# Kernel optimization log

Hardware: AMD Instinct MI355X
Metric: run time of the kernel (lower is better)

The kernel has to match this reference:

```python
import jax, jax.numpy as jnp
import numpy as np

NEG_BIG = -9e15


def setup_inputs() -> dict:
    key = jax.random.key(0)
    k1, k2, k3, k4 = jax.random.split(key, 4)
    B, N, F_in, F_out = 8, 2048, 512, 256
    x = jax.random.normal(k1, (B, N, F_in), dtype=jnp.float32)
    adj = jax.random.randint(k2, (B, N, N), 0, 2, dtype=jnp.int32)
    W = jax.random.normal(k3, (F_in, F_out), dtype=jnp.float32) * (1.414 / np.sqrt(F_in))
    a = jax.random.normal(k4, (2 * F_out, 1), dtype=jnp.float32) * 0.1
    return {"x": x, "adj": adj, "W": W, "a": a}


def reference(x, adj, W, a):
    # x: [B,N,Fin], adj: [B,N,N] int mask, W: [Fin,Fout], a: [2*Fout,1]
    alpha = 0.2  # LeakyReLU negative slope
    F_out = W.shape[1]
    h = jnp.einsum('bnf,fo->bno', x, W)              # [B,N,Fout]
    a1 = a[:F_out, 0]                                # [Fout]
    a2 = a[F_out:, 0]                                # [Fout]
    # e_ij = LeakyReLU([h_i || h_j] . a) = LeakyReLU(h_i.a1 + h_j.a2)
    f = h @ a1                                       # [B,N]
    g = h @ a2                                       # [B,N]
    e = jax.nn.leaky_relu(f[:, :, None] + g[:, None, :], negative_slope=alpha)  # [B,N,N]
    e = jnp.where(adj > 0, e, NEG_BIG)
    attention = jax.nn.softmax(e, axis=2)            # row-wise over neighbors j
    h_prime = jnp.einsum('bij,bjo->bio', attention, h)  # [B,N,Fout]
    return jax.nn.elu(h_prime)                       # concat=True path
```

## Files before the change

### kernel.cpp

```cpp
#include <hip/hip_runtime.h>
#include <hip/hip_bf16.h>
#include <math.h>

#define BATCH 8
#define NN    2048
#define FIN   512
#define FOUT  256
#define NEG_BIG -9000000000000000.0f

typedef __attribute__((ext_vector_type(8))) short bf16x8;
typedef __attribute__((ext_vector_type(4))) float f32x4;

__device__ __forceinline__ unsigned short f2bf(float x) {
    return __bfloat16_as_ushort(__float2bfloat16(x));
}
__device__ __forceinline__ float bf2f(unsigned short h) {
    return __uint_as_float(((unsigned)h) << 16);
}
__device__ __forceinline__ void gload_lds16(const void* g, void* l) {
    __builtin_amdgcn_global_load_lds((const __attribute__((address_space(1))) void*)g,
                                     (__attribute__((address_space(3))) void*)l,
                                     16, 0, 0);
}
__device__ __forceinline__ void lds_barrier() {
    asm volatile("s_waitcnt lgkmcnt(0)" ::: "memory");
    __builtin_amdgcn_s_barrier();
    asm volatile("" ::: "memory");
}

__global__ __launch_bounds__(256) void wt_prep(const float* __restrict__ W,
                                               unsigned short* __restrict__ Wtf_hi,
                                               unsigned short* __restrict__ Wtf_lo) {
    const int tg = blockIdx.x * 256 + threadIdx.x;
    const int n  = tg >> 7;
    const int k4 = (tg & 127) * 4;
    unsigned short h[4], lo[4];
    #pragma unroll
    for (int i = 0; i < 4; i++) {
        const float v = W[(size_t)(k4 + i) * FOUT + n];
        h[i]  = f2bf(v);
        lo[i] = f2bf(v - bf2f(h[i]));
    }
    const int ktile = k4 >> 5;
    const int ntile = n >> 4;
    const int lane  = ((k4 >> 3) & 3) * 16 + (n & 15);
    const size_t daddr = ((size_t)(ktile * 16 + ntile) * 64 + lane) * 8 + (k4 & 7);
    uint2 ph, pl;
    ph.x = h[0]  | ((unsigned)h[1]  << 16); ph.y = h[2]  | ((unsigned)h[3]  << 16);
    pl.x = lo[0] | ((unsigned)lo[1] << 16); pl.y = lo[2] | ((unsigned)lo[3] << 16);
    *(uint2*)(Wtf_hi + daddr) = ph;
    *(uint2*)(Wtf_lo + daddr) = pl;
}

__global__ __launch_bounds__(256, 2) void gemm_xw(const float* __restrict__ x,
        const unsigned short* __restrict__ Wtf_hi,
        const unsigned short* __restrict__ Wtf_lo,
        unsigned short* __restrict__ ht_hi,
        unsigned short* __restrict__ ht_lo) {
    __shared__ unsigned short As_hi[128][40];
    __shared__ unsigned short As_lo[128][40];
    __shared__ __attribute__((aligned(16))) unsigned short Tr[64][136];
    const int t  = threadIdx.x;
    const int m0 = (blockIdx.x >> 2) * 128;
    const int n0 = (blockIdx.x & 3) * 64;
    const int l  = t & 63, w = t >> 6;
    const int wr = w >> 1, wc = w & 1;
    const int lr = l & 15, lk = l >> 4;

    f32x4 acc[4][2];
    #pragma unroll
    for (int mt = 0; mt < 4; mt++)
        #pragma unroll
        for (int nt = 0; nt < 2; nt++) acc[mt][nt] = (f32x4){0.f,0.f,0.f,0.f};

    for (int k0 = 0; k0 < FIN; k0 += 32) {
        float4 xv[4];
        #pragma unroll
        for (int r = 0; r < 4; r++) {
            const int fidx = t + 256*r, m = fidx >> 3, kq = fidx & 7;
            xv[r] = *(const float4*)(x + (size_t)(m0 + m) * FIN + k0 + kq*4);
        }
        bf16x8 bh[2], bl[2];
        const size_t fb = ((size_t)((k0 >> 5) * 16 + (n0 >> 4) + wc*2) * 64 + l) * 8;
        #pragma unroll
        for (int nt = 0; nt < 2; nt++) {
            bh[nt] = *(const bf16x8*)(Wtf_hi + fb + (size_t)nt * 512);
            bl[nt] = *(const bf16x8*)(Wtf_lo + fb + (size_t)nt * 512);
        }
        __syncthreads();
        #pragma unroll
        for (int r = 0; r < 4; r++) {
            const int fidx = t + 256*r, m = fidx >> 3, kq = fidx & 7;
            const float vv[4] = {xv[r].x, xv[r].y, xv[r].z, xv[r].w};
            unsigned short h[4], lo[4];
            #pragma unroll
            for (int i = 0; i < 4; i++) { h[i] = f2bf(vv[i]); lo[i] = f2bf(vv[i] - bf2f(h[i])); }
            uint2 ph, pl;
            ph.x = h[0]  | ((unsigned)h[1]  << 16); ph.y = h[2]  | ((unsigned)h[3]  << 16);
            pl.x = lo[0] | ((unsigned)lo[1] << 16); pl.y = lo[2] | ((unsigned)lo[3] << 16);
            *(uint2*)&As_hi[m][kq*4] = ph;
            *(uint2*)&As_lo[m][kq*4] = pl;
        }
        __syncthreads();
        bf16x8 ah[4], al[4];
        #pragma unroll
        for (int mt = 0; mt < 4; mt++) {
            const int row = wr*64 + mt*16 + lr;
            ah[mt] = *(const bf16x8*)&As_hi[row][lk*8];
            al[mt] = *(const bf16x8*)&As_lo[row][lk*8];
        }
        #pragma unroll
        for (int nt = 0; nt < 2; nt++)
            #pragma unroll
            for (int mt = 0; mt < 4; mt++)
                acc[mt][nt] = __builtin_amdgcn_mfma_f32_16x16x32_bf16(ah[mt], bh[nt], acc[mt][nt], 0, 0, 0);
        #pragma unroll
        for (int nt = 0; nt < 2; nt++)
            #pragma unroll
            for (int mt = 0; mt < 4; mt++)
                acc[mt][nt] = __builtin_amdgcn_mfma_f32_16x16x32_bf16(ah[mt], bl[nt], acc[mt][nt], 0, 0, 0);
        #pragma unroll
        for (int nt = 0; nt < 2; nt++)
            #pragma unroll
            for (int mt = 0; mt < 4; mt++)
                acc[mt][nt] = __builtin_amdgcn_mfma_f32_16x16x32_bf16(al[mt], bh[nt], acc[mt][nt], 0, 0, 0);
    }

    const int bb  = m0 >> 11;
    const int jj0 = m0 & 2047;
    for (int pass = 0; pass < 2; pass++) {
        #pragma unroll
        for (int mt = 0; mt < 4; mt++)
            #pragma unroll
            for (int nt = 0; nt < 2; nt++) {
                const int nl = wc*32 + nt*16 + lr;
                const int ml = wr*64 + mt*16 + lk*4;
                const float vv[4] = {acc[mt][nt].x, acc[mt][nt].y, acc[mt][nt].z, acc[mt][nt].w};
                unsigned short s[4];
                #pragma unroll
                for (int r = 0; r < 4; r++) {
                    const unsigned short hh = f2bf(vv[r]);
                    s[r] = pass ? f2bf(vv[r] - bf2f(hh)) : hh;
                }
                *(unsigned*)&Tr[nl][ml]     = s[0] | ((unsigned)s[1] << 16);
                *(unsigned*)&Tr[nl][ml + 2] = s[2] | ((unsigned)s[3] << 16);
            }
        __syncthreads();
        unsigned short* dst = pass ? ht_lo : ht_hi;
        #pragma unroll
        for (int q = 0; q < 4; q++) {
            const int idx = t + 256*q, row = idx >> 4, c = idx & 15;
            *(uint4*)(dst + ((size_t)(bb * FOUT + n0 + row)) * NN + jj0 + c*8) =
                *(const uint4*)&Tr[row][c*8];
        }
        __syncthreads();
    }
}

__global__ __launch_bounds__(256) void fg2(const unsigned short* __restrict__ ht_hi,
                                           const unsigned short* __restrict__ ht_lo,
                                           const float* __restrict__ a,
                                           float* __restrict__ f, float* __restrict__ g) {
    __shared__ float Fp[4][64], Gp[4][64];
    const int lane = threadIdx.x & 63, wv = threadIdx.x >> 6;
    const int chunk = blockIdx.x;
    const int b  = chunk >> 5;
    const int jw = (chunk & 31) * 64 + lane;
    const size_t base = (size_t)b * FOUT * NN + jw;
    float fs = 0.f, gs = 0.f;
    #pragma unroll 4
    for (int n = wv*64; n < wv*64 + 64; n++) {
        const float hv = bf2f(ht_hi[base + (size_t)n * NN]) + bf2f(ht_lo[base + (size_t)n * NN]);
        fs = fmaf(hv, a[n], fs);
        gs = fmaf(hv, a[FOUT + n], gs);
    }
    Fp[wv][lane] = fs; Gp[wv][lane] = gs;
    __syncthreads();
    if (wv == 0) {
        f[b * NN + jw] = Fp[0][lane] + Fp[1][lane] + Fp[2][lane] + Fp[3][lane];
        g[b * NN + jw] = Gp[0][lane] + Gp[1][lane] + Gp[2][lane] + Gp[3][lane];
    }
}

__global__ __launch_bounds__(512, 1) void gat_attn(
        const unsigned short* __restrict__ ht_hi,
        const unsigned short* __restrict__ ht_lo,
        const int* __restrict__ adj,
        const float* __restrict__ f, const float* __restrict__ g,
        float* __restrict__ out) {
    __shared__ __attribute__((aligned(16))) unsigned short Hs_hi[2][16384];
    __shared__ __attribute__((aligned(16))) unsigned short Hs_lo[2][16384];
    __shared__ __attribute__((aligned(16))) unsigned short Ps_hi[4096];
    __shared__ __attribute__((aligned(16))) unsigned short Ps_lo[4096];
    __shared__ __attribute__((aligned(16))) float fac_s[64];
    __shared__ __attribute__((aligned(16))) float l_s[64];

    const int b  = blockIdx.x & 7;
    const int i0 = (blockIdx.x >> 3) * 64;
    const int t  = threadIdx.x;
    const int w  = t >> 6, l = t & 63;
    const int lr = l & 15, lk = l >> 4;
    const int wr = w >> 2, wc = w & 3;
    const int ar = t >> 3, jg = t & 7;

    const unsigned short* hb_hi = ht_hi + (size_t)b * FOUT * NN;
    const unsigned short* hb_lo = ht_lo + (size_t)b * FOUT * NN;
    const int*   adjr = adj + ((size_t)(b * NN + i0 + ar)) * NN + jg * 8;
    const float* gb   = g + b * NN + jg * 8;
    const float  fi   = f[b * NN + i0 + ar];

    float m_r = -INFINITY, l_r = 0.f;
    f32x4 acc[2][4] = {};
    const int slot = w * 4;

    int4 a0v, a1v; float4 g0v, g1v;

    auto STAGE = [&](int jt) {
        const int buf = jt & 1, j0 = jt * 64;
        #pragma unroll
        for (int q = 0; q < 4; q++) {
            const int idx = (slot + q) * 64 + l;
            const int n = idx >> 3, c = idx & 7;
            const int cc = c ^ (n & 7);
            const size_t go = (size_t)n * NN + j0 + cc * 8;
            gload_lds16(hb_hi + go, &Hs_hi[buf][(slot + q) * 512]);
            gload_lds16(hb_lo + go, &Hs_lo[buf][(slot + q) * 512]);
        }
    };
    auto LOADAG = [&](int jt) {
        const size_t jo = (size_t)jt * 64;
        a0v = *(const int4*)(adjr + jo);
        a1v = *(const int4*)(adjr + jo + 4);
        g0v = *(const float4*)(gb + jo);
        g1v = *(const float4*)(gb + jo + 4);
    };

    STAGE(0);
    asm volatile("" ::: "memory");
    LOADAG(0);

    for (int jt = 0; jt < 32; jt++) {
        const int buf = jt & 1;
        if (jt + 1 < 32) STAGE(jt + 1);
        asm volatile("" ::: "memory");

        {
            float p[8];
            {
                const float v0 = fi + g0v.x, v1 = fi + g0v.y, v2 = fi + g0v.z, v3 = fi + g0v.w;
                const float v4 = fi + g1v.x, v5 = fi + g1v.y, v6 = fi + g1v.z, v7 = fi + g1v.w;
                p[0] = a0v.x > 0 ? (v0 > 0.f ? v0 : 0.2f*v0) : NEG_BIG;
                p[1] = a0v.y > 0 ? (v1 > 0.f ? v1 : 0.2f*v1) : NEG_BIG;
                p[2] = a0v.z > 0 ? (v2 > 0.f ? v2 : 0.2f*v2) : NEG_BIG;
                p[3] = a0v.w > 0 ? (v3 > 0.f ? v3 : 0.2f*v3) : NEG_BIG;
                p[4] = a1v.x > 0 ? (v4 > 0.f ? v4 : 0.2f*v4) : NEG_BIG;
                p[5] = a1v.y > 0 ? (v5 > 0.f ? v5 : 0.2f*v5) : NEG_BIG;
                p[6] = a1v.z > 0 ? (v6 > 0.f ? v6 : 0.2f*v6) : NEG_BIG;
                p[7] = a1v.w > 0 ? (v7 > 0.f ? v7 : 0.2f*v7) : NEG_BIG;
            }
            float mloc = p[0];
            #pragma unroll
            for (int e = 1; e < 8; e++) mloc = fmaxf(mloc, p[e]);
            mloc = fmaxf(mloc, __shfl_xor(mloc, 1));
            mloc = fmaxf(mloc, __shfl_xor(mloc, 2));
            mloc = fmaxf(mloc, __shfl_xor(mloc, 4));
            const float mn = fmaxf(m_r, mloc);
            float rs = 0.f;
            #pragma unroll
            for (int e = 0; e < 8; e++) { p[e] = __expf(p[e] - mn); rs += p[e]; }
            rs += __shfl_xor(rs, 1);
            rs += __shfl_xor(rs, 2);
            rs += __shfl_xor(rs, 4);
            const float fac = __expf(m_r - mn);
            l_r = l_r * fac + rs;
            m_r = mn;
            if (jg == 0) { fac_s[ar] = fac; l_s[ar] = l_r; }
            unsigned hw_[4], lw_[4];
            #pragma unroll
            for (int e = 0; e < 8; e += 2) {
                const unsigned short h0 = f2bf(p[e]),   h1 = f2bf(p[e+1]);
                const unsigned short q0 = f2bf(p[e]   - bf2f(h0));
                const unsigned short q1 = f2bf(p[e+1] - bf2f(h1));
                hw_[e >> 1] = h0 | ((unsigned)h1 << 16);
                lw_[e >> 1] = q0 | ((unsigned)q1 << 16);
            }
            const int cs = (jg ^ (ar & 7)) * 8;
            *(uint4*)&Ps_hi[ar * 64 + cs] = make_uint4(hw_[0], hw_[1], hw_[2], hw_[3]);
            *(uint4*)&Ps_lo[ar * 64 + cs] = make_uint4(lw_[0], lw_[1], lw_[2], lw_[3]);
        }

        if (jt + 1 < 32) LOADAG(jt + 1);

        lds_barrier();

        #pragma unroll
        for (int mt = 0; mt < 2; mt++) {
            const f32x4 fac4 = *(const f32x4*)&fac_s[wr*32 + mt*16 + lk*4];
            #pragma unroll
            for (int nt = 0; nt < 4; nt++) acc[mt][nt] *= fac4;
        }
        __builtin_amdgcn_s_setprio(1);
        #pragma unroll
        for (int kt = 0; kt < 2; kt++) {
            bf16x8 ah[2], al[2], bh[4], bl[4];
            #pragma unroll
            for (int mt = 0; mt < 2; mt++) {
                const int row = wr*32 + mt*16 + lr;
                const int cs  = ((kt*4 + lk) ^ (row & 7)) * 8;
                ah[mt] = *(const bf16x8*)&Ps_hi[row * 64 + cs];
                al[mt] = *(const bf16x8*)&Ps_lo[row * 64 + cs];
            }
            #pragma unroll
            for (int nt = 0; nt < 4; nt++) {
                const int n  = wc*64 + nt*16 + lr;
                const int cs = ((kt*4 + lk) ^ (n & 7)) * 8;
                bh[nt] = *(const bf16x8*)&Hs_hi[buf][n * 64 + cs];
                bl[nt] = *(const bf16x8*)&Hs_lo[buf][n * 64 + cs];
            }
            #pragma unroll
            for (int nt = 0; nt < 4; nt++)
                #pragma unroll
                for (int mt = 0; mt < 2; mt++)
                    acc[mt][nt] = __builtin_amdgcn_mfma_f32_16x16x32_bf16(ah[mt], bh[nt], acc[mt][nt], 0, 0, 0);
            #pragma unroll
            for (int nt = 0; nt < 4; nt++)
                #pragma unroll
                for (int mt = 0; mt < 2; mt++)
                    acc[mt][nt] = __builtin_amdgcn_mfma_f32_16x16x32_bf16(ah[mt], bl[nt], acc[mt][nt], 0, 0, 0);
            #pragma unroll
            for (int nt = 0; nt < 4; nt++)
                #pragma unroll
                for (int mt = 0; mt < 2; mt++)
                    acc[mt][nt] = __builtin_amdgcn_mfma_f32_16x16x32_bf16(al[mt], bh[nt], acc[mt][nt], 0, 0, 0);
        }
        __builtin_amdgcn_s_setprio(0);

        lds_barrier();
    }

    #pragma unroll
    for (int mt = 0; mt < 2; mt++) {
        const f32x4 lv = *(const f32x4*)&l_s[wr*32 + mt*16 + lk*4];
        const float li[4] = {1.f/lv.x, 1.f/lv.y, 1.f/lv.z, 1.f/lv.w};
        #pragma unroll
        for (int nt = 0; nt < 4; nt++) {
            const int n = wc*64 + nt*16 + lr;
            const float av[4] = {acc[mt][nt].x, acc[mt][nt].y, acc[mt][nt].z, acc[mt][nt].w};
            #pragma unroll
            for (int r = 0; r < 4; r++) {
                float v = av[r] * li[r];
                v = v > 0.f ? v : (__expf(v) - 1.f);
                out[((size_t)(b * NN + i0 + wr*32 + mt*16 + lk*4 + r)) * FOUT + n] = v;
            }
        }
    }
}

extern "C" void kernel_launch(void* const* d_in, const int* in_sizes, int n_in,
                              void* d_out, int out_size, void* d_ws, size_t ws_size,
                              hipStream_t stream) {
    const float* x   = (const float*)d_in[0];
    const int*   adj = (const int*)  d_in[1];
    const float* W   = (const float*)d_in[2];
    const float* a   = (const float*)d_in[3];
    float* outp = (float*)d_out;

    char* ws = (char*)d_ws;
    unsigned short* ht_hi  = (unsigned short*)ws;                      ws += (size_t)BATCH*FOUT*NN*2;
    unsigned short* ht_lo  = (unsigned short*)ws;                      ws += (size_t)BATCH*FOUT*NN*2;
    unsigned short* Wtf_hi = (unsigned short*)ws;                      ws += (size_t)FOUT*FIN*2;
    unsigned short* Wtf_lo = (unsigned short*)ws;                      ws += (size_t)FOUT*FIN*2;
    float* f = (float*)ws;                                             ws += (size_t)BATCH*NN*4;
    float* g = (float*)ws;

    wt_prep <<<128, 256, 0, stream>>>(W, Wtf_hi, Wtf_lo);
    gemm_xw <<<512, 256, 0, stream>>>(x, Wtf_hi, Wtf_lo, ht_hi, ht_lo);
    fg2     <<<256, 256, 0, stream>>>(ht_hi, ht_lo, a, f, g);
    gat_attn<<<256, 512, 0, stream>>>(ht_hi, ht_lo, adj, f, g, outp);
}
```

Baseline: 287.3 us.

## Fuse f/g projection into GEMM epilogue and software-pipeline attention loop

The separate fg2 kernel is removed. f and g are now computed in the gemm_xw epilogue through shuffle reductions and atomicAdds into buffers zeroed by a memset. gemm_xw also loads x straight from global memory into MFMA fragments and drops the LDS staging and its barriers. The attention kernel is restructured so that the softmax phase for the next tile overlaps the MFMA work on the current tile, using an explicit vmcnt wait and a hoisted P fragment load. The atomics make the f/g sums order-dependent, and reading x without LDS staging may cost extra global traffic.

Result: slower. 299.4 us (+4.2%).

```diff
diff --git a/kernel.cpp b/kernel.cpp
--- a/kernel.cpp
+++ b/kernel.cpp
@@ -41,8 +41,7 @@
         h[i]  = f2bf(v);
         lo[i] = f2bf(v - bf2f(h[i]));
     }
-    const int ktile = k4 >> 5;
-    const int ntile = n >> 4;
+    const int ktile = k4 >> 5, ntile = n >> 4;
     const int lane  = ((k4 >> 3) & 3) * 16 + (n & 15);
     const size_t daddr = ((size_t)(ktile * 16 + ntile) * 64 + lane) * 8 + (k4 & 7);
     uint2 ph, pl;
@@ -55,10 +54,10 @@
 __global__ __launch_bounds__(256, 2) void gemm_xw(const float* __restrict__ x,
         const unsigned short* __restrict__ Wtf_hi,
         const unsigned short* __restrict__ Wtf_lo,
+        const float* __restrict__ a,
         unsigned short* __restrict__ ht_hi,
-        unsigned short* __restrict__ ht_lo) {
-    __shared__ unsigned short As_hi[128][40];
-    __shared__ unsigned short As_lo[128][40];
+        unsigned short* __restrict__ ht_lo,
+        float* __restrict__ f, float* __restrict__ g) {
     __shared__ __attribute__((aligned(16))) unsigned short Tr[64][136];
     const int t  = threadIdx.x;
     const int m0 = (blockIdx.x >> 2) * 128;
@@ -73,13 +72,9 @@
         #pragma unroll
         for (int nt = 0; nt < 2; nt++) acc[mt][nt] = (f32x4){0.f,0.f,0.f,0.f};
 
+    const float* xw = x + (size_t)(m0 + wr*64 + lr) * FIN + lk*8;
+
     for (int k0 = 0; k0 < FIN; k0 += 32) {
-        float4 xv[4];
-        #pragma unroll
-        for (int r = 0; r < 4; r++) {
-            const int fidx = t + 256*r, m = fidx >> 3, kq = fidx & 7;
-            xv[r] = *(const float4*)(x + (size_t)(m0 + m) * FIN + k0 + kq*4);
-        }
         bf16x8 bh[2], bl[2];
         const size_t fb = ((size_t)((k0 >> 5) * 16 + (n0 >> 4) + wc*2) * 64 + l) * 8;
         #pragma unroll
@@ -87,27 +82,18 @@
             bh[nt] = *(const bf16x8*)(Wtf_hi + fb + (size_t)nt * 512);
             bl[nt] = *(const bf16x8*)(Wtf_lo + fb + (size_t)nt * 512);
         }
-        __syncthreads();
-        #pragma unroll
-        for (int r = 0; r < 4; r++) {
-            const int fidx = t + 256*r, m = fidx >> 3, kq = fidx & 7;
-            const float vv[4] = {xv[r].x, xv[r].y, xv[r].z, xv[r].w};
-            unsigned short h[4], lo[4];
-            #pragma unroll
-            for (int i = 0; i < 4; i++) { h[i] = f2bf(vv[i]); lo[i] = f2bf(vv[i] - bf2f(h[i])); }
-            uint2 ph, pl;
-            ph.x = h[0]  | ((unsigned)h[1]  << 16); ph.y = h[2]  | ((unsigned)h[3]  << 16);
-            pl.x = lo[0] | ((unsigned)lo[1] << 16); pl.y = lo[2] | ((unsigned)lo[3] << 16);
-            *(uint2*)&As_hi[m][kq*4] = ph;
-            *(uint2*)&As_lo[m][kq*4] = pl;
-        }
-        __syncthreads();
         bf16x8 ah[4], al[4];
         #pragma unroll
         for (int mt = 0; mt < 4; mt++) {
-            const int row = wr*64 + mt*16 + lr;
-            ah[mt] = *(const bf16x8*)&As_hi[row][lk*8];
-            al[mt] = *(const bf16x8*)&As_lo[row][lk*8];
+            const float4 v0 = *(const float4*)(xw + (size_t)mt*16*FIN + k0);
+            const float4 v1 = *(const float4*)(xw + (size_t)mt*16*FIN + k0 + 4);
+            const float vv[8] = {v0.x,v0.y,v0.z,v0.w,v1.x,v1.y,v1.z,v1.w};
+            #pragma unroll
+            for (int e = 0; e < 8; e++) {
+                const unsigned short hh = f2bf(vv[e]);
+                ah[mt][e] = (short)hh;
+                al[mt][e] = (short)f2bf(vv[e] - bf2f(hh));
+            }
         }
         #pragma unroll
         for (int nt = 0; nt < 2; nt++)
@@ -128,6 +114,32 @@
 
     const int bb  = m0 >> 11;
     const int jj0 = m0 & 2047;
+
+    {
+        const int nA = n0 + wc*32 + lr;
+        const float a1A = a[nA],        a1B = a[nA + 16];
+        const float a2A = a[FOUT + nA], a2B = a[FOUT + nA + 16];
+        #pragma unroll
+        for (int mt = 0; mt < 4; mt++) {
+            #pragma unroll
+            for (int r = 0; r < 4; r++) {
+                float fp = acc[mt][0][r] * a1A + acc[mt][1][r] * a1B;
+                float gp = acc[mt][0][r] * a2A + acc[mt][1][r] * a2B;
+                #pragma unroll
+                for (int m = 1; m < 16; m <<= 1) {
+                    fp += __shfl_xor(fp, m);
+                    gp += __shfl_xor(gp, m);
+                }
+                if (lr == 0) {
+                    const int row = m0 + wr*64 + mt*16 + lk*4 + r;
+                    const int jj  = row & 2047;
+                    atomicAdd(&f[(size_t)bb * NN + jj], fp);
+                    atomicAdd(&g[(size_t)bb * NN + jj], gp);
+                }
+            }
+        }
+    }
+
     for (int pass = 0; pass < 2; pass++) {
         #pragma unroll
         for (int mt = 0; mt < 4; mt++)
@@ -154,31 +166,6 @@
                 *(const uint4*)&Tr[row][c*8];
         }
         __syncthreads();
-    }
-}
-
-__global__ __launch_bounds__(256) void fg2(const unsigned short* __restrict__ ht_hi,
-                                           const unsigned short* __restrict__ ht_lo,
-                                           const float* __restrict__ a,
-                                           float* __restrict__ f, float* __restrict__ g) {
-    __shared__ float Fp[4][64], Gp[4][64];
-    const int lane = threadIdx.x & 63, wv = threadIdx.x >> 6;
-    const int chunk = blockIdx.x;
-    const int b  = chunk >> 5;
-    const int jw = (chunk & 31) * 64 + lane;
-    const size_t base = (size_t)b * FOUT * NN + jw;
-    float fs = 0.f, gs = 0.f;
-    #pragma unroll 4
-    for (int n = wv*64; n < wv*64 + 64; n++) {
-        const float hv = bf2f(ht_hi[base + (size_t)n * NN]) + bf2f(ht_lo[base + (size_t)n * NN]);
-        fs = fmaf(hv, a[n], fs);
-        gs = fmaf(hv, a[FOUT + n], gs);
-    }
-    Fp[wv][lane] = fs; Gp[wv][lane] = gs;
-    __syncthreads();
-    if (wv == 0) {
-        f[b * NN + jw] = Fp[0][lane] + Fp[1][lane] + Fp[2][lane] + Fp[3][lane];
-        g[b * NN + jw] = Gp[0][lane] + Gp[1][lane] + Gp[2][lane] + Gp[3][lane];
     }
 }
 
@@ -234,82 +221,54 @@
         g0v = *(const float4*)(gb + jo);
         g1v = *(const float4*)(gb + jo + 4);
     };
-
-    STAGE(0);
-    asm volatile("" ::: "memory");
-    LOADAG(0);
-
-    for (int jt = 0; jt < 32; jt++) {
-        const int buf = jt & 1;
-        if (jt + 1 < 32) STAGE(jt + 1);
-        asm volatile("" ::: "memory");
-
+    auto PHASE_A = [&]() {
+        float p[8];
         {
-            float p[8];
-            {
-                const float v0 = fi + g0v.x, v1 = fi + g0v.y, v2 = fi + g0v.z, v3 = fi + g0v.w;
-                const float v4 = fi + g1v.x, v5 = fi + g1v.y, v6 = fi + g1v.z, v7 = fi + g1v.w;
-                p[0] = a0v.x > 0 ? (v0 > 0.f ? v0 : 0.2f*v0) : NEG_BIG;
-                p[1] = a0v.y > 0 ? (v1 > 0.f ? v1 : 0.2f*v1) : NEG_BIG;
-                p[2] = a0v.z > 0 ? (v2 > 0.f ? v2 : 0.2f*v2) : NEG_BIG;
-                p[3] = a0v.w > 0 ? (v3 > 0.f ? v3 : 0.2f*v3) : NEG_BIG;
-                p[4] = a1v.x > 0 ? (v4 > 0.f ? v4 : 0.2f*v4) : NEG_BIG;
-                p[5] = a1v.y > 0 ? (v5 > 0.f ? v5 : 0.2f*v5) : NEG_BIG;
-                p[6] = a1v.z > 0 ? (v6 > 0.f ? v6 : 0.2f*v6) : NEG_BIG;
-                p[7] = a1v.w > 0 ? (v7 > 0.f ? v7 : 0.2f*v7) : NEG_BIG;
-            }
-            float mloc = p[0];
-            #pragma unroll
-            for (int e = 1; e < 8; e++) mloc = fmaxf(mloc, p[e]);
-            mloc = fmaxf(mloc, __shfl_xor(mloc, 1));
-            mloc = fmaxf(mloc, __shfl_xor(mloc, 2));
-            mloc = fmaxf(mloc, __shfl_xor(mloc, 4));
-            const float mn = fmaxf(m_r, mloc);
-            float rs = 0.f;
-            #pragma unroll
-            for (int e = 0; e < 8; e++) { p[e] = __expf(p[e] - mn); rs += p[e]; }
-            rs += __shfl_xor(rs, 1);
-            rs += __shfl_xor(rs, 2);
-            rs += __shfl_xor(rs, 4);
-            const float fac = __expf(m_r - mn);
-            l_r = l_r * fac + rs;
-            m_r = mn;
-            if (jg == 0) { fac_s[ar] = fac; l_s[ar] = l_r; }
-            unsigned hw_[4], lw_[4];
-            #pragma unroll
-            for (int e = 0; e < 8; e += 2) {
-                const unsigned short h0 = f2bf(p[e]),   h1 = f2bf(p[e+1]);
-                const unsigned short q0 = f2bf(p[e]   - bf2f(h0));
-                const unsigned short q1 = f2bf(p[e+1] - bf2f(h1));
-                hw_[e >> 1] = h0 | ((unsigned)h1 << 16);
-                lw_[e >> 1] = q0 | ((unsigned)q1 << 16);
-            }
-            const int cs = (jg ^ (ar & 7)) * 8;
-            *(uint4*)&Ps_hi[ar * 64 + cs] = make_uint4(hw_[0], hw_[1], hw_[2], hw_[3]);
-            *(uint4*)&Ps_lo[ar * 64 + cs] = make_uint4(lw_[0], lw_[1], lw_[2], lw_[3]);
-        }
-
-        if (jt + 1 < 32) LOADAG(jt + 1);
-
-        lds_barrier();
-
-        #pragma unroll
-        for (int mt = 0; mt < 2; mt++) {
-            const f32x4 fac4 = *(const f32x4*)&fac_s[wr*32 + mt*16 + lk*4];
-            #pragma unroll
-            for (int nt = 0; nt < 4; nt++) acc[mt][nt] *= fac4;
-        }
-        __builtin_amdgcn_s_setprio(1);
+            const float v0 = fi + g0v.x, v1 = fi + g0v.y, v2 = fi + g0v.z, v3 = fi + g0v.w;
+            const float v4 = fi + g1v.x, v5 = fi + g1v.y, v6 = fi + g1v.z, v7 = fi + g1v.w;
+            p[0] = a0v.x > 0 ? (v0 > 0.f ? v0 : 0.2f*v0) : NEG_BIG;
+            p[1] = a0v.y > 0 ? (v1 > 0.f ? v1 : 0.2f*v1) : NEG_BIG;
+            p[2] = a0v.z > 0 ? (v2 > 0.f ? v2 : 0.2f*v2) : NEG_BIG;
+            p[3] = a0v.w > 0 ? (v3 > 0.f ? v3 : 0.2f*v3) : NEG_BIG;
+            p[4] = a1v.x > 0 ? (v4 > 0.f ? v4 : 0.2f*v4) : NEG_BIG;
+            p[5] = a1v.y > 0 ? (v5 > 0.f ? v5 : 0.2f*v5) : NEG_BIG;
+            p[6] = a1v.z > 0 ? (v6 > 0.f ? v6 : 0.2f*v6) : NEG_BIG;
+            p[7] = a1v.w > 0 ? (v7 > 0.f ? v7 : 0.2f*v7) : NEG_BIG;
+        }
+        float mloc = p[0];
+        #pragma unroll
+        for (int e = 1; e < 8; e++) mloc = fmaxf(mloc, p[e]);
+        mloc = fmaxf(mloc, __shfl_xor(mloc, 1));
+        mloc = fmaxf(mloc, __shfl_xor(mloc, 2));
+        mloc = fmaxf(mloc, __shfl_xor(mloc, 4));
+        const float mn = fmaxf(m_r, mloc);
+        float rs = 0.f;
+        #pragma unroll
+        for (int e = 0; e < 8; e++) { p[e] = __expf(p[e] - mn); rs += p[e]; }
+        rs += __shfl_xor(rs, 1);
+        rs += __shfl_xor(rs, 2);
+        rs += __shfl_xor(rs, 4);
+        const float fac = __expf(m_r - mn);
+        l_r = l_r * fac + rs;
+        m_r = mn;
+        if (jg == 0) { fac_s[ar] = fac; l_s[ar] = l_r; }
+        unsigned hw_[4], lw_[4];
+        #pragma unroll
+        for (int e = 0; e < 8; e += 2) {
+            const unsigned short h0 = f2bf(p[e]),   h1 = f2bf(p[e+1]);
+            const unsigned short q0 = f2bf(p[e]   - bf2f(h0));
+            const unsigned short q1 = f2bf(p[e+1] - bf2f(h1));
+            hw_[e >> 1] = h0 | ((unsigned)h1 << 16);
+            lw_[e >> 1] = q0 | ((unsigned)q1 << 16);
+        }
+        const int cs = (jg ^ (ar & 7)) * 8;
+        *(uint4*)&Ps_hi[ar * 64 + cs] = make_uint4(hw_[0], hw_[1], hw_[2], hw_[3]);
+        *(uint4*)&Ps_lo[ar * 64 + cs] = make_uint4(lw_[0], lw_[1], lw_[2], lw_[3]);
+    };
+    auto MFMA_TILE = [&](int buf, const bf16x8 (&ahf)[2][2], const bf16x8 (&alf)[2][2]) {
         #pragma unroll
         for (int kt = 0; kt < 2; kt++) {
-            bf16x8 ah[2], al[2], bh[4], bl[4];
-            #pragma unroll
-            for (int mt = 0; mt < 2; mt++) {
-                const int row = wr*32 + mt*16 + lr;
-                const int cs  = ((kt*4 + lk) ^ (row & 7)) * 8;
-                ah[mt] = *(const bf16x8*)&Ps_hi[row * 64 + cs];
-                al[mt] = *(const bf16x8*)&Ps_lo[row * 64 + cs];
-            }
+            bf16x8 bh[4], bl[4];
             #pragma unroll
             for (int nt = 0; nt < 4; nt++) {
                 const int n  = wc*64 + nt*16 + lr;
@@ -321,21 +280,76 @@
             for (int nt = 0; nt < 4; nt++)
                 #pragma unroll
                 for (int mt = 0; mt < 2; mt++)
-                    acc[mt][nt] = __builtin_amdgcn_mfma_f32_16x16x32_bf16(ah[mt], bh[nt], acc[mt][nt], 0, 0, 0);
+                    acc[mt][nt] = __builtin_amdgcn_mfma_f32_16x16x32_bf16(ahf[mt][kt], bh[nt], acc[mt][nt], 0, 0, 0);
             #pragma unroll
             for (int nt = 0; nt < 4; nt++)
                 #pragma unroll
                 for (int mt = 0; mt < 2; mt++)
-                    acc[mt][nt] = __builtin_amdgcn_mfma_f32_16x16x32_bf16(ah[mt], bl[nt], acc[mt][nt], 0, 0, 0);
+                    acc[mt][nt] = __builtin_amdgcn_mfma_f32_16x16x32_bf16(ahf[mt][kt], bl[nt], acc[mt][nt], 0, 0, 0);
             #pragma unroll
             for (int nt = 0; nt < 4; nt++)
                 #pragma unroll
                 for (int mt = 0; mt < 2; mt++)
-                    acc[mt][nt] = __builtin_amdgcn_mfma_f32_16x16x32_bf16(al[mt], bh[nt], acc[mt][nt], 0, 0, 0);
-        }
-        __builtin_amdgcn_s_setprio(0);
-
+                    acc[mt][nt] = __builtin_amdgcn_mfma_f32_16x16x32_bf16(alf[mt][kt], bh[nt], acc[mt][nt], 0, 0, 0);
+        }
+    };
+
+    STAGE(0);
+    LOADAG(0);
+    PHASE_A();
+    LOADAG(1);
+    lds_barrier();
+
+    bf16x8 ahf[2][2], alf[2][2];
+    f32x4 fac4[2];
+
+    for (int jt = 0; jt < 31; jt++) {
+        const int buf = jt & 1;
+        STAGE(jt + 1);
+        asm volatile("s_waitcnt vmcnt(8)" ::: "memory");
+        __builtin_amdgcn_sched_barrier(0);
+        #pragma unroll
+        for (int mt = 0; mt < 2; mt++) {
+            fac4[mt] = *(const f32x4*)&fac_s[wr*32 + mt*16 + lk*4];
+            #pragma unroll
+            for (int kt = 0; kt < 2; kt++) {
+                const int row = wr*32 + mt*16 + lr;
+                const int cs  = ((kt*4 + lk) ^ (row & 7)) * 8;
+                ahf[mt][kt] = *(const bf16x8*)&Ps_hi[row * 64 + cs];
+                alf[mt][kt] = *(const bf16x8*)&Ps_lo[row * 64 + cs];
+            }
+        }
         lds_barrier();
+        #pragma unroll
+        for (int mt = 0; mt < 2; mt++)
+            #pragma unroll
+            for (int nt = 0; nt < 4; nt++) acc[mt][nt] *= fac4[mt];
+        PHASE_A();
+        if (jt < 30) LOADAG(jt + 2);
+        MFMA_TILE(buf, ahf, alf);
+        lds_barrier();
+    }
+
+    {
+        asm volatile("s_waitcnt vmcnt(0)" ::: "memory");
+        __builtin_amdgcn_sched_barrier(0);
+        #pragma unroll
+        for (int mt = 0; mt < 2; mt++) {
+            fac4[mt] = *(const f32x4*)&fac_s[wr*32 + mt*16 + lk*4];
+            #pragma unroll
+            for (int kt = 0; kt < 2; kt++) {
+                const int row = wr*32 + mt*16 + lr;
+                const int cs  = ((kt*4 + lk) ^ (row & 7)) * 8;
+                ahf[mt][kt] = *(const bf16x8*)&Ps_hi[row * 64 + cs];
+                alf[mt][kt] = *(const bf16x8*)&Ps_lo[row * 64 + cs];
+            }
+        }
+        lds_barrier();
+        #pragma unroll
+        for (int mt = 0; mt < 2; mt++)
+            #pragma unroll
+            for (int nt = 0; nt < 4; nt++) acc[mt][nt] *= fac4[mt];
+        MFMA_TILE(1, ahf, alf);
     }
 
     #pragma unroll
@@ -373,8 +387,8 @@
     float* f = (float*)ws;                                             ws += (size_t)BATCH*NN*4;
     float* g = (float*)ws;
 
+    hipMemsetAsync(f, 0, (size_t)2 * BATCH * NN * 4, stream);
     wt_prep <<<128, 256, 0, stream>>>(W, Wtf_hi, Wtf_lo);
-    gemm_xw <<<512, 256, 0, stream>>>(x, Wtf_hi, Wtf_lo, ht_hi, ht_lo);
-    fg2     <<<256, 256, 0, stream>>>(ht_hi, ht_lo, a, f, g);
+    gemm_xw <<<512, 256, 0, stream>>>(x, Wtf_hi, Wtf_lo, a, ht_hi, ht_lo, f, g);
     gat_attn<<<256, 512, 0, stream>>>(ht_hi, ht_lo, adj, f, g, outp);
 }
```
